# Kernel tuning notes

Hardware: AMD Instinct MI355X
Metric: run time of the kernel (lower is better)

## Reference

```python
import jax, jax.numpy as jnp
import numpy as np

HEADS = 4
C = 128            # per-head out channels (hard-coded 128 in the module)
NEG_SLOPE_ATT = 0.2   # GATConv attention leaky_relu slope
NEG_SLOPE = 0.01      # F.leaky_relu default slope


def _diag_output_ids(num_groups, n):
    # ids = base_i + n*j + j for group i, agent j; base_i = i * n^2
    i = np.arange(num_groups)[:, None] * (n * n)
    j = np.arange(n)[None, :] * (n + 1)
    return jnp.asarray((i + j).reshape(-1))


def setup_inputs() -> dict:
    key = jax.random.key(0)
    ks = jax.random.split(key, 12)
    num_groups, n_agents = 12, 48
    N = num_groups * n_agents * n_agents      # 27648 nodes
    E = 442368
    F_in, edge_dim, hidden = 256, 16, 256
    s = 0.05
    return {
        "x": jax.random.normal(ks[0], (N, F_in), jnp.float32),
        "edge_index": jax.random.randint(ks[1], (2, E), 0, N, jnp.int32),
        "edge_attr": jax.random.normal(ks[2], (E, edge_dim), jnp.float32),
        "num_groups": num_groups,
        "agents_per_group": n_agents,
        "W": jax.random.normal(ks[3], (F_in, HEADS * C), jnp.float32) * s,
        "att_src": jax.random.normal(ks[4], (HEADS, C), jnp.float32) * s,
        "att_dst": jax.random.normal(ks[5], (HEADS, C), jnp.float32) * s,
        "W_edge": jax.random.normal(ks[6], (edge_dim, HEADS * C), jnp.float32) * s,
        "att_edge": jax.random.normal(ks[7], (HEADS, C), jnp.float32) * s,
        "bias_gat": jnp.zeros((HEADS * C,), jnp.float32),
        "fc_W": jax.random.normal(ks[8], (HEADS * C, hidden), jnp.float32) * s,
        "fc_b": jnp.zeros((hidden,), jnp.float32),
    }


def _gat_conv(x, src, dst, edge_attr_full, W, att_src, att_dst, W_edge, att_edge, bias):
    N = x.shape[0]
    h = (x @ W).reshape(N, HEADS, C)                       # [N,H,C]
    a_src = jnp.einsum('nhc,hc->nh', h, att_src)           # [N,H]
    a_dst = jnp.einsum('nhc,hc->nh', h, att_dst)
    he = (edge_attr_full @ W_edge).reshape(-1, HEADS, C)   # [E',H,C]
    a_edge = jnp.einsum('ehc,hc->eh', he, att_edge)
    logits = jax.nn.leaky_relu(a_src[src] + a_dst[dst] + a_edge, NEG_SLOPE_ATT)
    # segment softmax over incoming edges of each dst node
    m = jax.ops.segment_max(logits, dst, num_segments=N)   # [N,H]
    e = jnp.exp(logits - m[dst])
    s = jax.ops.segment_sum(e, dst, num_segments=N)
    alpha = e / (s[dst] + 1e-16)                           # [E',H]
    msg = h[src] * alpha[..., None]                        # [E',H,C]
    out = jax.ops.segment_sum(msg, dst, num_segments=N)    # [N,H,C]
    return out.reshape(N, HEADS * C) + bias


def reference(x, edge_index, edge_attr, num_groups, agents_per_group,
              W, att_src, att_dst, W_edge, att_edge, bias_gat, fc_W, fc_b):
    N = x.shape[0]
    # add self-loops (PyG default), self-loop edge_attr = mean fill
    loops = jnp.arange(N, dtype=edge_index.dtype)
    src = jnp.concatenate([edge_index[0], loops])
    dst = jnp.concatenate([edge_index[1], loops])
    ea = jnp.concatenate([edge_attr,
                          jnp.broadcast_to(edge_attr.mean(0), (N, edge_attr.shape[1]))])
    h = jax.nn.leaky_relu(
        _gat_conv(x, src, dst, ea, W, att_src, att_dst, W_edge, att_edge, bias_gat),
        NEG_SLOPE)
    ids = _diag_output_ids(num_groups, agents_per_group)
    # fc_output + leaky_relu then diagonal index-select (select first: same math)
    return jax.nn.leaky_relu(h[ids] @ fc_W + fc_b, NEG_SLOPE)
```

## Files before the change

### kernel.cpp

```cpp
#include <hip/hip_runtime.h>

#define NNODES 27648
#define NEDGES 442368
#define FIN    256
#define HC     512
#define NH     4
#define CDIM   128
#define NAG    48
#define NGRP   12
#define N2     2304
#define NOUT   576
#define CAP    128
#define EDIM   16
#define MPART  512
#define BINB0  (9 + MPART)
#define PREB   (BINB0 + NEDGES/256)


__device__ __forceinline__ float lrelu(float v, float s){ return v > 0.0f ? v : s * v; }

__device__ __forceinline__ float wsum(float v){
  #pragma unroll
  for (int off = 32; off; off >>= 1) v += __shfl_xor(v, off, 64);
  return v;
}
__device__ __forceinline__ float wmax(float v){
  #pragma unroll
  for (int off = 32; off; off >>= 1) v = fmaxf(v, __shfl_xor(v, off, 64));
  return v;
}

__global__ __launch_bounds__(256) void k_pre(
    const float* __restrict__ W, const float* __restrict__ att_src,
    const float* __restrict__ att_dst, const float* __restrict__ W_edge,
    const float* __restrict__ att_edge, const float* __restrict__ ea,
    const int* __restrict__ ei,
    float* __restrict__ ws_, float* __restrict__ wd_, float* __restrict__ we_,
    float* __restrict__ easum, int* __restrict__ counts, int* __restrict__ slist){
  int b = blockIdx.x;
  int tid = threadIdx.x;
  if (b < 9) {
    int g = b * 256 + tid;
    if (g < 1024) {
      int f = g >> 2, h = g & 3;
      const float4* wp = (const float4*)(W + f*HC + h*CDIM);
      const float4* ap = (const float4*)(att_src + h*CDIM);
      float s = 0.f;
      #pragma unroll 8
      for (int c4 = 0; c4 < CDIM/4; c4++){
        float4 wv = wp[c4], av = ap[c4];
        s += wv.x*av.x + wv.y*av.y + wv.z*av.z + wv.w*av.w;
      }
      ws_[g] = s;
    } else if (g < 2048) {
      int gg = g - 1024; int f = gg >> 2, h = gg & 3;
      const float4* wp = (const float4*)(W + f*HC + h*CDIM);
      const float4* ap = (const float4*)(att_dst + h*CDIM);
      float s = 0.f;
      #pragma unroll 8
      for (int c4 = 0; c4 < CDIM/4; c4++){
        float4 wv = wp[c4], av = ap[c4];
        s += wv.x*av.x + wv.y*av.y + wv.z*av.z + wv.w*av.w;
      }
      wd_[gg] = s;
    } else if (g < 2112) {
      int gg = g - 2048; int d = gg >> 2, h = gg & 3;
      const float4* wp = (const float4*)(W_edge + d*HC + h*CDIM);
      const float4* ap = (const float4*)(att_edge + h*CDIM);
      float s = 0.f;
      #pragma unroll 8
      for (int c4 = 0; c4 < CDIM/4; c4++){
        float4 wv = wp[c4], av = ap[c4];
        s += wv.x*av.x + wv.y*av.y + wv.z*av.z + wv.w*av.w;
      }
      we_[gg] = s;
    }
  } else if (b < BINB0) {
    int pb = b - 9;
    const float4* p = (const float4*)ea;
    const int total = NEDGES * 4;
    float4 acc = make_float4(0.f, 0.f, 0.f, 0.f);
    for (int i = pb*256 + tid; i < total; i += MPART*256){
      float4 v = p[i];
      acc.x += v.x; acc.y += v.y; acc.z += v.z; acc.w += v.w;
    }
    #pragma unroll
    for (int off = 4; off <= 32; off <<= 1){
      acc.x += __shfl_xor(acc.x, off, 64);
      acc.y += __shfl_xor(acc.y, off, 64);
      acc.z += __shfl_xor(acc.z, off, 64);
      acc.w += __shfl_xor(acc.w, off, 64);
    }
    __shared__ float4 sd4[16];
    int lane = tid & 63, wave = tid >> 6;
    if (lane < 4) sd4[wave*4 + lane] = acc;
    __syncthreads();
    if (tid < 4){
      float4 t = sd4[tid];
      float4 a = sd4[4+tid], c = sd4[8+tid], d = sd4[12+tid];
      t.x += a.x + c.x + d.x; t.y += a.y + c.y + d.y;
      t.z += a.z + c.z + d.z; t.w += a.w + c.w + d.w;
      atomicAdd(&easum[4*tid+0], t.x);
      atomicAdd(&easum[4*tid+1], t.y);
      atomicAdd(&easum[4*tid+2], t.z);
      atomicAdd(&easum[4*tid+3], t.w);
    }
  } else {
    int e = (b - BINB0)*256 + tid;
    int dst = ei[NEDGES + e];
    int r = dst % N2;
    if (r % 49) return;
    int row = (dst / N2) * NAG + r / 49;
    int pos = atomicAdd(&counts[row], 1);
    if (pos >= CAP) return;
    slist[row*CAP + pos] = e;
  }
}

__global__ __launch_bounds__(256) void k_attn(const float* __restrict__ x,
    const int* __restrict__ ei, const float* __restrict__ ea,
    const float* __restrict__ ws_, const float* __restrict__ wd_,
    const float* __restrict__ we_, const float* __restrict__ easum,
    const int* __restrict__ counts, const int* __restrict__ slist,
    float* __restrict__ z){
  __shared__ float  lg[(CAP+1)*4];
  __shared__ int    srcs[CAP+1];
  __shared__ float  adst_s[4];
  __shared__ float4 pz[4*256];
  int row = blockIdx.x;
  int tid = threadIdx.x;
  int lane = tid & 63, wave = tid >> 6;
  int k = counts[row]; if (k > CAP) k = CAP;
  int g = row / NAG, j = row - g*NAG;
  int dst = g*N2 + j*49;

  float wsr[4][4];
  #pragma unroll
  for (int q = 0; q < 4; q++){
    float4 t = *(const float4*)(ws_ + (lane*4+q)*4);
    wsr[q][0]=t.x; wsr[q][1]=t.y; wsr[q][2]=t.z; wsr[q][3]=t.w;
  }
  float4 we4 = (lane < 16) ? *(const float4*)(we_ + lane*4)
                           : make_float4(0.f,0.f,0.f,0.f);

  for (int i = wave; i < k; i += 4){
    int e = slist[row*CAP + i];
    int src = ei[e];
    float eav = (lane < 16) ? ea[(size_t)e*EDIM + lane] : 0.f;
    float4 xv = *(const float4*)(x + (size_t)src*FIN + lane*4);
    float p0 = xv.x*wsr[0][0] + xv.y*wsr[1][0] + xv.z*wsr[2][0] + xv.w*wsr[3][0] + eav*we4.x;
    float p1 = xv.x*wsr[0][1] + xv.y*wsr[1][1] + xv.z*wsr[2][1] + xv.w*wsr[3][1] + eav*we4.y;
    float p2 = xv.x*wsr[0][2] + xv.y*wsr[1][2] + xv.z*wsr[2][2] + xv.w*wsr[3][2] + eav*we4.z;
    float p3 = xv.x*wsr[0][3] + xv.y*wsr[1][3] + xv.z*wsr[2][3] + xv.w*wsr[3][3] + eav*we4.w;
    p0 = wsum(p0); p1 = wsum(p1); p2 = wsum(p2); p3 = wsum(p3);
    if (lane == 0){
      srcs[i] = src;
      lg[i*4+0] = p0; lg[i*4+1] = p1; lg[i*4+2] = p2; lg[i*4+3] = p3;
    }
  }

  if (wave == 0){
    float wdr[4][4];
    #pragma unroll
    for (int q = 0; q < 4; q++){
      float4 t = *(const float4*)(wd_ + (lane*4+q)*4);
      wdr[q][0]=t.x; wdr[q][1]=t.y; wdr[q][2]=t.z; wdr[q][3]=t.w;
    }
    float4 xv = *(const float4*)(x + (size_t)dst*FIN + lane*4);
    const float invE = 1.0f/(float)NEDGES;
    float c = (lane < 16) ? easum[lane]*invE : 0.f;
    float ps[4], pd[4];
    ps[0] = xv.x*wsr[0][0] + xv.y*wsr[1][0] + xv.z*wsr[2][0] + xv.w*wsr[3][0] + c*we4.x;
    ps[1] = xv.x*wsr[0][1] + xv.y*wsr[1][1] + xv.z*wsr[2][1] + xv.w*wsr[3][1] + c*we4.y;
    ps[2] = xv.x*wsr[0][2] + xv.y*wsr[1][2] + xv.z*wsr[2][2] + xv.w*wsr[3][2] + c*we4.z;
    ps[3] = xv.x*wsr[0][3] + xv.y*wsr[1][3] + xv.z*wsr[2][3] + xv.w*wsr[3][3] + c*we4.w;
    #pragma unroll
    for (int h = 0; h < 4; h++){
      pd[h] = xv.x*wdr[0][h] + xv.y*wdr[1][h] + xv.z*wdr[2][h] + xv.w*wdr[3][h];
      ps[h] = wsum(ps[h]);
      pd[h] = wsum(pd[h]);
    }
    if (lane == 0){
      #pragma unroll
      for (int h = 0; h < 4; h++){
        adst_s[h] = pd[h];
        lg[k*4+h] = ps[h];
      }
      srcs[k] = dst;
    }
  }
  __syncthreads();

  {
    int h = wave;
    float ad = adst_s[h];
    float m = -1e30f;
    for (int i = lane; i <= k; i += 64){
      float v = lrelu(lg[i*4+h] + ad, 0.2f);
      lg[i*4+h] = v;
      m = fmaxf(m, v);
    }
    m = wmax(m);
    float s = 0.f;
    for (int i = lane; i <= k; i += 64){
      float e = __expf(lg[i*4+h] - m);
      lg[i*4+h] = e;
      s += e;
    }
    s = wsum(s);
    float inv = 1.0f/(s + 1e-16f);
    for (int i = lane; i <= k; i += 64) lg[i*4+h] *= inv;
  }
  __syncthreads();

  {
    float acc[4][4];
    #pragma unroll
    for (int h = 0; h < 4; h++)
      #pragma unroll
      for (int c = 0; c < 4; c++) acc[h][c] = 0.f;
    for (int i = wave; i <= k; i += 4){
      int src = srcs[i];
      float4 xv = *(const float4*)(x + (size_t)src*FIN + lane*4);
      float a0 = lg[i*4+0], a1 = lg[i*4+1], a2 = lg[i*4+2], a3 = lg[i*4+3];
      acc[0][0] += a0*xv.x; acc[0][1] += a0*xv.y; acc[0][2] += a0*xv.z; acc[0][3] += a0*xv.w;
      acc[1][0] += a1*xv.x; acc[1][1] += a1*xv.y; acc[1][2] += a1*xv.z; acc[1][3] += a1*xv.w;
      acc[2][0] += a2*xv.x; acc[2][1] += a2*xv.y; acc[2][2] += a2*xv.z; acc[2][3] += a2*xv.w;
      acc[3][0] += a3*xv.x; acc[3][1] += a3*xv.y; acc[3][2] += a3*xv.z; acc[3][3] += a3*xv.w;
    }
    #pragma unroll
    for (int h = 0; h < 4; h++)
      pz[wave*256 + h*64 + lane] =
        make_float4(acc[h][0], acc[h][1], acc[h][2], acc[h][3]);
  }
  __syncthreads();
  {
    float4 a = pz[tid], b = pz[256+tid], c = pz[512+tid], d = pz[768+tid];
    ((float4*)(z + (size_t)row*1024))[tid] =
      make_float4(a.x+b.x+c.x+d.x, a.y+b.y+c.y+d.y,
                  a.z+b.z+c.z+d.z, a.w+b.w+c.w+d.w);
  }
}

__global__ __launch_bounds__(256) void k_gemm1(const float* __restrict__ z,
    const float* __restrict__ W, const float* __restrict__ bias,
    float* __restrict__ h2){
  __shared__ float  zt[256][8];
  __shared__ float4 part[8][8][32];
  int rb = blockIdx.x * 8;
  int h  = blockIdx.y;
  int tid = threadIdx.x;
  for (int idx = tid; idx < 2048; idx += 256){
    int r = idx >> 8, f = idx & 255;
    zt[f][r] = z[(size_t)(rb+r)*1024 + h*256 + f];
  }
  __syncthreads();
  {
    int cg = tid & 31, q = tid >> 5;
    const float4* Wp = (const float4*)(W + h*CDIM) + cg;
    float4 acc[8];
    #pragma unroll
    for (int r = 0; r < 8; r++) acc[r] = make_float4(0.f,0.f,0.f,0.f);
    int f0 = q*32;
    #pragma unroll 8
    for (int jf = 0; jf < 32; jf++){
      int f = f0 + jf;
      float4 w4 = Wp[(size_t)f*(HC/4)];
      float4 zlo = *(const float4*)&zt[f][0];
      float4 zhi = *(const float4*)&zt[f][4];
      acc[0].x += zlo.x*w4.x; acc[0].y += zlo.x*w4.y; acc[0].z += zlo.x*w4.z; acc[0].w += zlo.x*w4.w;
      acc[1].x += zlo.y*w4.x; acc[1].y += zlo.y*w4.y; acc[1].z += zlo.y*w4.z; acc[1].w += zlo.y*w4.w;
      acc[2].x += zlo.z*w4.x; acc[2].y += zlo.z*w4.y; acc[2].z += zlo.z*w4.z; acc[2].w += zlo.z*w4.w;
      acc[3].x += zlo.w*w4.x; acc[3].y += zlo.w*w4.y; acc[3].z += zlo.w*w4.z; acc[3].w += zlo.w*w4.w;
      acc[4].x += zhi.x*w4.x; acc[4].y += zhi.x*w4.y; acc[4].z += zhi.x*w4.z; acc[4].w += zhi.x*w4.w;
      acc[5].x += zhi.y*w4.x; acc[5].y += zhi.y*w4.y; acc[5].z += zhi.y*w4.z; acc[5].w += zhi.y*w4.w;
      acc[6].x += zhi.z*w4.x; acc[6].y += zhi.z*w4.y; acc[6].z += zhi.z*w4.z; acc[6].w += zhi.z*w4.w;
      acc[7].x += zhi.w*w4.x; acc[7].y += zhi.w*w4.y; acc[7].z += zhi.w*w4.z; acc[7].w += zhi.w*w4.w;
    }
    #pragma unroll
    for (int r = 0; r < 8; r++) part[q][r][cg] = acc[r];
  }
  __syncthreads();
  {
    int r = tid >> 5, cg = tid & 31;
    float4 s0 = part[0][r][cg];
    #pragma unroll
    for (int q = 1; q < 8; q++){
      float4 t = part[q][r][cg];
      s0.x += t.x; s0.y += t.y; s0.z += t.z; s0.w += t.w;
    }
    float4 bs = ((const float4*)bias)[h*32 + cg];
    float4 o;
    o.x = lrelu(s0.x+bs.x, 0.01f);
    o.y = lrelu(s0.y+bs.y, 0.01f);
    o.z = lrelu(s0.z+bs.z, 0.01f);
    o.w = lrelu(s0.w+bs.w, 0.01f);
    *(float4*)(h2 + (size_t)(rb+r)*HC + h*CDIM + 4*cg) = o;
  }
}

__global__ __launch_bounds__(256) void k_gemm2(const float* __restrict__ h2,
    const float* __restrict__ fcW, const float* __restrict__ fcb,
    float* __restrict__ out){
  __shared__ float  ht[512][8];
  __shared__ float4 part[16][8][16];
  int rb = blockIdx.x * 8;
  int cb = blockIdx.y;
  int tid = threadIdx.x;
  for (int idx = tid; idx < 4096; idx += 256){
    int r = idx >> 9, kf = idx & 511;
    ht[kf][r] = h2[(size_t)(rb+r)*HC + kf];
  }
  __syncthreads();
  {
    int cg = tid & 15, q = tid >> 4;
    const float4* Fp = (const float4*)(fcW + cb*64) + cg;
    float4 acc[8];
    #pragma unroll
    for (int r = 0; r < 8; r++) acc[r] = make_float4(0.f,0.f,0.f,0.f);
    int k0 = q*32;
    #pragma unroll 8
    for (int jk = 0; jk < 32; jk++){
      int kf = k0 + jk;
      float4 w4 = Fp[(size_t)kf*64];
      float4 hlo = *(const float4*)&ht[kf][0];
      float4 hhi = *(const float4*)&ht[kf][4];
      acc[0].x += hlo.x*w4.x; acc[0].y += hlo.x*w4.y; acc[0].z += hlo.x*w4.z; acc[0].w += hlo.x*w4.w;
      acc[1].x += hlo.y*w4.x; acc[1].y += hlo.y*w4.y; acc[1].z += hlo.y*w4.z; acc[1].w += hlo.y*w4.w;
      acc[2].x += hlo.z*w4.x; acc[2].y += hlo.z*w4.y; acc[2].z += hlo.z*w4.z; acc[2].w += hlo.z*w4.w;
      acc[3].x += hlo.w*w4.x; acc[3].y += hlo.w*w4.y; acc[3].z += hlo.w*w4.z; acc[3].w += hlo.w*w4.w;
      acc[4].x += hhi.x*w4.x; acc[4].y += hhi.x*w4.y; acc[4].z += hhi.x*w4.z; acc[4].w += hhi.x*w4.w;
      acc[5].x += hhi.y*w4.x; acc[5].y += hhi.y*w4.y; acc[5].z += hhi.y*w4.z; acc[5].w += hhi.y*w4.w;
      acc[6].x += hhi.z*w4.x; acc[6].y += hhi.z*w4.y; acc[6].z += hhi.z*w4.z; acc[6].w += hhi.z*w4.w;
      acc[7].x += hhi.w*w4.x; acc[7].y += hhi.w*w4.y; acc[7].z += hhi.w*w4.z; acc[7].w += hhi.w*w4.w;
    }
    #pragma unroll
    for (int r = 0; r < 8; r++) part[q][r][cg] = acc[r];
  }
  __syncthreads();
  if (tid < 128){
    int r = tid >> 4, cg = tid & 15;
    float4 s0 = part[0][r][cg];
    #pragma unroll
    for (int q = 1; q < 16; q++){
      float4 t = part[q][r][cg];
      s0.x += t.x; s0.y += t.y; s0.z += t.z; s0.w += t.w;
    }
    float4 bs = ((const float4*)fcb)[cb*16 + cg];
    float4 o;
    o.x = lrelu(s0.x+bs.x, 0.01f);
    o.y = lrelu(s0.y+bs.y, 0.01f);
    o.z = lrelu(s0.z+bs.z, 0.01f);
    o.w = lrelu(s0.w+bs.w, 0.01f);
    *(float4*)(out + (size_t)(rb+r)*256 + cb*64 + 4*cg) = o;
  }
}

extern "C" void kernel_launch(void* const* d_in, const int* in_sizes, int n_in,
                              void* d_out, int out_size, void* d_ws, size_t ws_size,
                              hipStream_t stream) {
  const float* x        = (const float*)d_in[0];
  const int*   ei       = (const int*)  d_in[1];
  const float* ea       = (const float*)d_in[2];
  const float* W        = (const float*)d_in[5];
  const float* att_src  = (const float*)d_in[6];
  const float* att_dst  = (const float*)d_in[7];
  const float* W_edge   = (const float*)d_in[8];
  const float* att_edge = (const float*)d_in[9];
  const float* bias     = (const float*)d_in[10];
  const float* fcW      = (const float*)d_in[11];
  const float* fcb      = (const float*)d_in[12];
  float* out = (float*)d_out;

  float* w = (float*)d_ws;
  float*  ws_       = w;
  float*  wd_       = w + 1024;
  float*  we_       = w + 2048;
  float*  easum     = w + 2112;
  int*    counts    = (int*)(w + 2128);
  int*    slist     = (int*)(w + 2704);
  float*  z         = w + 76432;
  float*  h2        = w + 666256;

  hipMemsetAsync(easum, 0, (16 + NOUT)*sizeof(float), stream);
  k_pre<<<PREB, 256, 0, stream>>>(W, att_src, att_dst, W_edge, att_edge, ea, ei,
                                  ws_, wd_, we_, easum, counts, slist);
  k_attn<<<NOUT, 256, 0, stream>>>(x, ei, ea, ws_, wd_, we_, easum,
                                   counts, slist, z);
  k_gemm1<<<dim3(NOUT/8, 4), 256, 0, stream>>>(z, W, bias, h2);
  k_gemm2<<<dim3(NOUT/8, 4), 256, 0, stream>>>(h2, fcW, fcb, out);
}
```

Measured before the change: 167.9 us.

## Split edge binning into scan kernel, precompute edge logits, widen attention blocks

The memset is removed: counts are now zeroed inside k_pre, and the edge_attr sum is written as per-block partials instead of using atomics. A new k_scan kernel bins edges by destination, stores the source id directly, and precomputes the per-edge attention term from edge_attr, while one extra block reduces the partial sums. k_attn runs with 512 threads (8 waves) and reads the precomputed edge logits, which removes the indirect ei/ea gathers. In exchange this adds a kernel launch and a serial dependency, and the 8-way partial reduction makes shared memory larger.

```diff
diff --git a/kernel.cpp b/kernel.cpp
--- a/kernel.cpp
+++ b/kernel.cpp
@@ -13,8 +13,6 @@
 #define CAP    128
 #define EDIM   16
 #define MPART  512
-#define BINB0  (9 + MPART)
-#define PREB   (BINB0 + NEDGES/256)
 
 
 __device__ __forceinline__ float lrelu(float v, float s){ return v > 0.0f ? v : s * v; }
@@ -34,12 +32,11 @@
     const float* __restrict__ W, const float* __restrict__ att_src,
     const float* __restrict__ att_dst, const float* __restrict__ W_edge,
     const float* __restrict__ att_edge, const float* __restrict__ ea,
-    const int* __restrict__ ei,
     float* __restrict__ ws_, float* __restrict__ wd_, float* __restrict__ we_,
-    float* __restrict__ easum, int* __restrict__ counts, int* __restrict__ slist){
+    int* __restrict__ counts, float4* __restrict__ easum_part){
   int b = blockIdx.x;
   int tid = threadIdx.x;
-  if (b < 9) {
+  if (b < 11) {
     int g = b * 256 + tid;
     if (g < 1024) {
       int f = g >> 2, h = g & 3;
@@ -74,9 +71,11 @@
         s += wv.x*av.x + wv.y*av.y + wv.z*av.z + wv.w*av.w;
       }
       we_[gg] = s;
-    }
-  } else if (b < BINB0) {
-    int pb = b - 9;
+    } else if (g < 2112 + NOUT) {
+      counts[g - 2112] = 0;
+    }
+  } else {
+    int pb = b - 11;
     const float4* p = (const float4*)ea;
     const int total = NEDGES * 4;
     float4 acc = make_float4(0.f, 0.f, 0.f, 0.f);
@@ -100,33 +99,60 @@
       float4 a = sd4[4+tid], c = sd4[8+tid], d = sd4[12+tid];
       t.x += a.x + c.x + d.x; t.y += a.y + c.y + d.y;
       t.z += a.z + c.z + d.z; t.w += a.w + c.w + d.w;
-      atomicAdd(&easum[4*tid+0], t.x);
-      atomicAdd(&easum[4*tid+1], t.y);
-      atomicAdd(&easum[4*tid+2], t.z);
-      atomicAdd(&easum[4*tid+3], t.w);
-    }
-  } else {
-    int e = (b - BINB0)*256 + tid;
-    int dst = ei[NEDGES + e];
-    int r = dst % N2;
-    if (r % 49) return;
-    int row = (dst / N2) * NAG + r / 49;
-    int pos = atomicAdd(&counts[row], 1);
-    if (pos >= CAP) return;
-    slist[row*CAP + pos] = e;
-  }
-}
-
-__global__ __launch_bounds__(256) void k_attn(const float* __restrict__ x,
-    const int* __restrict__ ei, const float* __restrict__ ea,
+      easum_part[pb*4 + tid] = t;
+    }
+  }
+}
+
+__global__ __launch_bounds__(256) void k_scan(const int* __restrict__ ei,
+    const float* __restrict__ ea, const float* __restrict__ we_,
+    int* __restrict__ counts, int* __restrict__ slist, float* __restrict__ aed,
+    const float* __restrict__ easum_part, float* __restrict__ easum){
+  int tid = threadIdx.x;
+  if (blockIdx.x == NEDGES/256){
+    int col = tid & 15, part = tid >> 4;
+    float s = 0.f;
+    for (int pb = 0; pb < MPART/16; pb++)
+      s += easum_part[(part*(MPART/16) + pb)*16 + col];
+    __shared__ float sd[256];
+    sd[tid] = s;
+    __syncthreads();
+    if (tid < 16){
+      float t = 0.f;
+      #pragma unroll
+      for (int i = 0; i < 16; i++) t += sd[i*16 + tid];
+      easum[tid] = t;
+    }
+    return;
+  }
+  int e = blockIdx.x*256 + tid;
+  int dst = ei[NEDGES + e];
+  int r = dst % N2;
+  if (r % 49) return;
+  int row = (dst / N2) * NAG + r / 49;
+  int pos = atomicAdd(&counts[row], 1);
+  if (pos >= CAP) return;
+  slist[row*CAP + pos] = ei[e];
+  const float* eap = ea + (size_t)e*EDIM;
+  float a0=0.f,a1=0.f,a2=0.f,a3=0.f;
+  #pragma unroll
+  for (int d = 0; d < EDIM; d++){
+    float v = eap[d];
+    a0 += v*we_[d*4+0]; a1 += v*we_[d*4+1]; a2 += v*we_[d*4+2]; a3 += v*we_[d*4+3];
+  }
+  float* ap = aed + (size_t)(row*CAP+pos)*4;
+  ap[0]=a0; ap[1]=a1; ap[2]=a2; ap[3]=a3;
+}
+
+__global__ __launch_bounds__(512) void k_attn(const float* __restrict__ x,
     const float* __restrict__ ws_, const float* __restrict__ wd_,
     const float* __restrict__ we_, const float* __restrict__ easum,
     const int* __restrict__ counts, const int* __restrict__ slist,
-    float* __restrict__ z){
+    const float* __restrict__ aed, float* __restrict__ z){
   __shared__ float  lg[(CAP+1)*4];
   __shared__ int    srcs[CAP+1];
   __shared__ float  adst_s[4];
-  __shared__ float4 pz[4*256];
+  __shared__ float4 pz[8*256];
   int row = blockIdx.x;
   int tid = threadIdx.x;
   int lane = tid & 63, wave = tid >> 6;
@@ -140,22 +166,20 @@
     float4 t = *(const float4*)(ws_ + (lane*4+q)*4);
     wsr[q][0]=t.x; wsr[q][1]=t.y; wsr[q][2]=t.z; wsr[q][3]=t.w;
   }
-  float4 we4 = (lane < 16) ? *(const float4*)(we_ + lane*4)
-                           : make_float4(0.f,0.f,0.f,0.f);
-
-  for (int i = wave; i < k; i += 4){
-    int e = slist[row*CAP + i];
-    int src = ei[e];
-    float eav = (lane < 16) ? ea[(size_t)e*EDIM + lane] : 0.f;
+
+  for (int i = wave; i < k; i += 8){
+    int src = slist[row*CAP + i];
+    float4 aedv = *(const float4*)(aed + (size_t)(row*CAP+i)*4);
     float4 xv = *(const float4*)(x + (size_t)src*FIN + lane*4);
-    float p0 = xv.x*wsr[0][0] + xv.y*wsr[1][0] + xv.z*wsr[2][0] + xv.w*wsr[3][0] + eav*we4.x;
-    float p1 = xv.x*wsr[0][1] + xv.y*wsr[1][1] + xv.z*wsr[2][1] + xv.w*wsr[3][1] + eav*we4.y;
-    float p2 = xv.x*wsr[0][2] + xv.y*wsr[1][2] + xv.z*wsr[2][2] + xv.w*wsr[3][2] + eav*we4.z;
-    float p3 = xv.x*wsr[0][3] + xv.y*wsr[1][3] + xv.z*wsr[2][3] + xv.w*wsr[3][3] + eav*we4.w;
+    float p0 = xv.x*wsr[0][0] + xv.y*wsr[1][0] + xv.z*wsr[2][0] + xv.w*wsr[3][0];
+    float p1 = xv.x*wsr[0][1] + xv.y*wsr[1][1] + xv.z*wsr[2][1] + xv.w*wsr[3][1];
+    float p2 = xv.x*wsr[0][2] + xv.y*wsr[1][2] + xv.z*wsr[2][2] + xv.w*wsr[3][2];
+    float p3 = xv.x*wsr[0][3] + xv.y*wsr[1][3] + xv.z*wsr[2][3] + xv.w*wsr[3][3];
     p0 = wsum(p0); p1 = wsum(p1); p2 = wsum(p2); p3 = wsum(p3);
     if (lane == 0){
       srcs[i] = src;
-      lg[i*4+0] = p0; lg[i*4+1] = p1; lg[i*4+2] = p2; lg[i*4+3] = p3;
+      lg[i*4+0] = p0 + aedv.x; lg[i*4+1] = p1 + aedv.y;
+      lg[i*4+2] = p2 + aedv.z; lg[i*4+3] = p3 + aedv.w;
     }
   }
 
@@ -167,31 +191,34 @@
       wdr[q][0]=t.x; wdr[q][1]=t.y; wdr[q][2]=t.z; wdr[q][3]=t.w;
     }
     float4 xv = *(const float4*)(x + (size_t)dst*FIN + lane*4);
-    const float invE = 1.0f/(float)NEDGES;
-    float c = (lane < 16) ? easum[lane]*invE : 0.f;
-    float ps[4], pd[4];
-    ps[0] = xv.x*wsr[0][0] + xv.y*wsr[1][0] + xv.z*wsr[2][0] + xv.w*wsr[3][0] + c*we4.x;
-    ps[1] = xv.x*wsr[0][1] + xv.y*wsr[1][1] + xv.z*wsr[2][1] + xv.w*wsr[3][1] + c*we4.y;
-    ps[2] = xv.x*wsr[0][2] + xv.y*wsr[1][2] + xv.z*wsr[2][2] + xv.w*wsr[3][2] + c*we4.z;
-    ps[3] = xv.x*wsr[0][3] + xv.y*wsr[1][3] + xv.z*wsr[2][3] + xv.w*wsr[3][3] + c*we4.w;
+    float pd[4], ps[4];
     #pragma unroll
     for (int h = 0; h < 4; h++){
       pd[h] = xv.x*wdr[0][h] + xv.y*wdr[1][h] + xv.z*wdr[2][h] + xv.w*wdr[3][h];
+      ps[h] = xv.x*wsr[0][h] + xv.y*wsr[1][h] + xv.z*wsr[2][h] + xv.w*wsr[3][h];
+    }
+    const float invE = 1.0f/(float)NEDGES;
+    float md = (lane < 16) ? easum[lane]*invE : 0.f;
+    float al[4];
+    #pragma unroll
+    for (int h = 0; h < 4; h++){
+      float c = (lane < 16) ? md*we_[lane*4+h] : 0.f;
+      al[h] = wsum(c);
+      pd[h] = wsum(pd[h]);
       ps[h] = wsum(ps[h]);
-      pd[h] = wsum(pd[h]);
     }
     if (lane == 0){
       #pragma unroll
       for (int h = 0; h < 4; h++){
         adst_s[h] = pd[h];
-        lg[k*4+h] = ps[h];
+        lg[k*4+h] = ps[h] + al[h];
       }
       srcs[k] = dst;
     }
   }
   __syncthreads();
 
-  {
+  if (wave < 4){
     int h = wave;
     float ad = adst_s[h];
     float m = -1e30f;
@@ -219,7 +246,7 @@
     for (int h = 0; h < 4; h++)
       #pragma unroll
       for (int c = 0; c < 4; c++) acc[h][c] = 0.f;
-    for (int i = wave; i <= k; i += 4){
+    for (int i = wave; i <= k; i += 8){
       int src = srcs[i];
       float4 xv = *(const float4*)(x + (size_t)src*FIN + lane*4);
       float a0 = lg[i*4+0], a1 = lg[i*4+1], a2 = lg[i*4+2], a3 = lg[i*4+3];
@@ -234,11 +261,14 @@
         make_float4(acc[h][0], acc[h][1], acc[h][2], acc[h][3]);
   }
   __syncthreads();
-  {
-    float4 a = pz[tid], b = pz[256+tid], c = pz[512+tid], d = pz[768+tid];
-    ((float4*)(z + (size_t)row*1024))[tid] =
-      make_float4(a.x+b.x+c.x+d.x, a.y+b.y+c.y+d.y,
-                  a.z+b.z+c.z+d.z, a.w+b.w+c.w+d.w);
+  if (tid < 256){
+    float4 s0 = pz[tid];
+    #pragma unroll
+    for (int w = 1; w < 8; w++){
+      float4 t = pz[w*256 + tid];
+      s0.x += t.x; s0.y += t.y; s0.z += t.z; s0.w += t.w;
+    }
+    ((float4*)(z + (size_t)row*1024))[tid] = s0;
   }
 }
 
@@ -378,15 +408,17 @@
   float*  we_       = w + 2048;
   float*  easum     = w + 2112;
   int*    counts    = (int*)(w + 2128);
-  int*    slist     = (int*)(w + 2704);
-  float*  z         = w + 76432;
-  float*  h2        = w + 666256;
-
-  hipMemsetAsync(easum, 0, (16 + NOUT)*sizeof(float), stream);
-  k_pre<<<PREB, 256, 0, stream>>>(W, att_src, att_dst, W_edge, att_edge, ea, ei,
-                                  ws_, wd_, we_, easum, counts, slist);
-  k_attn<<<NOUT, 256, 0, stream>>>(x, ei, ea, ws_, wd_, we_, easum,
-                                   counts, slist, z);
+  float*  easum_p   = w + 2704;
+  int*    slist     = (int*)(w + 10896);
+  float*  aed       = w + 84624;
+  float*  z         = w + 379536;
+  float*  h2        = w + 969360;
+
+  k_pre<<<11 + MPART, 256, 0, stream>>>(W, att_src, att_dst, W_edge, att_edge, ea,
+                                        ws_, wd_, we_, counts, (float4*)easum_p);
+  k_scan<<<NEDGES/256 + 1, 256, 0, stream>>>(ei, ea, we_, counts, slist, aed,
+                                             easum_p, easum);
+  k_attn<<<NOUT, 512, 0, stream>>>(x, ws_, wd_, we_, easum, counts, slist, aed, z);
   k_gemm1<<<dim3(NOUT/8, 4), 256, 0, stream>>>(z, W, bias, h2);
   k_gemm2<<<dim3(NOUT/8, 4), 256, 0, stream>>>(h2, fcW, fcb, out);
 }
```

After: 147.1 us, median of 2. -12.4%, faster.

## Double attention block width and precompute edge logits per edge in a batched pass

Applied to the files above, without the earlier changes.

The attention kernel now runs 512 threads (8 waves) per output row instead of 256. Each incoming edge's source index and edge-attribute logit contribution are computed once, one thread per edge, in a cooperative prologue and staged in shared memory. The gather loops then stride over 8 waves, and the final reduction sums 8 partial accumulators. This aims to expose more memory-level parallelism for the x-row gathers and to remove the serialized per-edge slist/ei/ea loads from the wave loop, at the cost of extra barriers, more shared memory and fewer blocks per CU.

```diff
diff --git a/kernel.cpp b/kernel.cpp
--- a/kernel.cpp
+++ b/kernel.cpp
@@ -13,8 +13,9 @@
 #define CAP    128
 #define EDIM   16
 #define MPART  512
-#define BINB0  (9 + MPART)
-#define PREB   (BINB0 + NEDGES/256)
+#define PRE_WB 9
+#define PRE_EB (PRE_WB + MPART)
+#define PREB   (PRE_EB + NEDGES/256)
 
 
 __device__ __forceinline__ float lrelu(float v, float s){ return v > 0.0f ? v : s * v; }
@@ -39,7 +40,7 @@
     float* __restrict__ easum, int* __restrict__ counts, int* __restrict__ slist){
   int b = blockIdx.x;
   int tid = threadIdx.x;
-  if (b < 9) {
+  if (b < PRE_WB) {
     int g = b * 256 + tid;
     if (g < 1024) {
       int f = g >> 2, h = g & 3;
@@ -75,8 +76,8 @@
       }
       we_[gg] = s;
     }
-  } else if (b < BINB0) {
-    int pb = b - 9;
+  } else if (b < PRE_EB) {
+    int pb = b - PRE_WB;
     const float4* p = (const float4*)ea;
     const int total = NEDGES * 4;
     float4 acc = make_float4(0.f, 0.f, 0.f, 0.f);
@@ -106,7 +107,7 @@
       atomicAdd(&easum[4*tid+3], t.w);
     }
   } else {
-    int e = (b - BINB0)*256 + tid;
+    int e = (b - PRE_EB)*256 + tid;
     int dst = ei[NEDGES + e];
     int r = dst % N2;
     if (r % 49) return;
@@ -117,7 +118,7 @@
   }
 }
 
-__global__ __launch_bounds__(256) void k_attn(const float* __restrict__ x,
+__global__ __launch_bounds__(512) void k_attn(const float* __restrict__ x,
     const int* __restrict__ ei, const float* __restrict__ ea,
     const float* __restrict__ ws_, const float* __restrict__ wd_,
     const float* __restrict__ we_, const float* __restrict__ easum,
@@ -126,7 +127,9 @@
   __shared__ float  lg[(CAP+1)*4];
   __shared__ int    srcs[CAP+1];
   __shared__ float  adst_s[4];
-  __shared__ float4 pz[4*256];
+  __shared__ float  wesh[64];
+  __shared__ float4 aedsh[CAP];
+  __shared__ float4 pz[8*256];
   int row = blockIdx.x;
   int tid = threadIdx.x;
   int lane = tid & 63, wave = tid >> 6;
@@ -134,28 +137,46 @@
   int g = row / NAG, j = row - g*NAG;
   int dst = g*N2 + j*49;
 
+  if (tid < 64) wesh[tid] = we_[tid];
+  __syncthreads();
+
+  if (tid < k){
+    int e = slist[row*CAP + tid];
+    int src = ei[e];
+    const float4* eap = (const float4*)(ea + (size_t)e*EDIM);
+    float4 e0 = eap[0], e1 = eap[1], e2 = eap[2], e3 = eap[3];
+    float a[4];
+    #pragma unroll
+    for (int h = 0; h < 4; h++){
+      a[h] = e0.x*wesh[0*4+h]  + e0.y*wesh[1*4+h]  + e0.z*wesh[2*4+h]  + e0.w*wesh[3*4+h]
+           + e1.x*wesh[4*4+h]  + e1.y*wesh[5*4+h]  + e1.z*wesh[6*4+h]  + e1.w*wesh[7*4+h]
+           + e2.x*wesh[8*4+h]  + e2.y*wesh[9*4+h]  + e2.z*wesh[10*4+h] + e2.w*wesh[11*4+h]
+           + e3.x*wesh[12*4+h] + e3.y*wesh[13*4+h] + e3.z*wesh[14*4+h] + e3.w*wesh[15*4+h];
+    }
+    srcs[tid] = src;
+    aedsh[tid] = make_float4(a[0], a[1], a[2], a[3]);
+  }
+  __syncthreads();
+
   float wsr[4][4];
   #pragma unroll
   for (int q = 0; q < 4; q++){
     float4 t = *(const float4*)(ws_ + (lane*4+q)*4);
     wsr[q][0]=t.x; wsr[q][1]=t.y; wsr[q][2]=t.z; wsr[q][3]=t.w;
   }
-  float4 we4 = (lane < 16) ? *(const float4*)(we_ + lane*4)
-                           : make_float4(0.f,0.f,0.f,0.f);
-
-  for (int i = wave; i < k; i += 4){
-    int e = slist[row*CAP + i];
-    int src = ei[e];
-    float eav = (lane < 16) ? ea[(size_t)e*EDIM + lane] : 0.f;
+
+  for (int i = wave; i < k; i += 8){
+    int src = srcs[i];
+    float4 aedv = aedsh[i];
     float4 xv = *(const float4*)(x + (size_t)src*FIN + lane*4);
-    float p0 = xv.x*wsr[0][0] + xv.y*wsr[1][0] + xv.z*wsr[2][0] + xv.w*wsr[3][0] + eav*we4.x;
-    float p1 = xv.x*wsr[0][1] + xv.y*wsr[1][1] + xv.z*wsr[2][1] + xv.w*wsr[3][1] + eav*we4.y;
-    float p2 = xv.x*wsr[0][2] + xv.y*wsr[1][2] + xv.z*wsr[2][2] + xv.w*wsr[3][2] + eav*we4.z;
-    float p3 = xv.x*wsr[0][3] + xv.y*wsr[1][3] + xv.z*wsr[2][3] + xv.w*wsr[3][3] + eav*we4.w;
+    float p0 = xv.x*wsr[0][0] + xv.y*wsr[1][0] + xv.z*wsr[2][0] + xv.w*wsr[3][0];
+    float p1 = xv.x*wsr[0][1] + xv.y*wsr[1][1] + xv.z*wsr[2][1] + xv.w*wsr[3][1];
+    float p2 = xv.x*wsr[0][2] + xv.y*wsr[1][2] + xv.z*wsr[2][2] + xv.w*wsr[3][2];
+    float p3 = xv.x*wsr[0][3] + xv.y*wsr[1][3] + xv.z*wsr[2][3] + xv.w*wsr[3][3];
     p0 = wsum(p0); p1 = wsum(p1); p2 = wsum(p2); p3 = wsum(p3);
     if (lane == 0){
-      srcs[i] = src;
-      lg[i*4+0] = p0; lg[i*4+1] = p1; lg[i*4+2] = p2; lg[i*4+3] = p3;
+      lg[i*4+0] = p0 + aedv.x; lg[i*4+1] = p1 + aedv.y;
+      lg[i*4+2] = p2 + aedv.z; lg[i*4+3] = p3 + aedv.w;
     }
   }
 
@@ -167,31 +188,34 @@
       wdr[q][0]=t.x; wdr[q][1]=t.y; wdr[q][2]=t.z; wdr[q][3]=t.w;
     }
     float4 xv = *(const float4*)(x + (size_t)dst*FIN + lane*4);
-    const float invE = 1.0f/(float)NEDGES;
-    float c = (lane < 16) ? easum[lane]*invE : 0.f;
-    float ps[4], pd[4];
-    ps[0] = xv.x*wsr[0][0] + xv.y*wsr[1][0] + xv.z*wsr[2][0] + xv.w*wsr[3][0] + c*we4.x;
-    ps[1] = xv.x*wsr[0][1] + xv.y*wsr[1][1] + xv.z*wsr[2][1] + xv.w*wsr[3][1] + c*we4.y;
-    ps[2] = xv.x*wsr[0][2] + xv.y*wsr[1][2] + xv.z*wsr[2][2] + xv.w*wsr[3][2] + c*we4.z;
-    ps[3] = xv.x*wsr[0][3] + xv.y*wsr[1][3] + xv.z*wsr[2][3] + xv.w*wsr[3][3] + c*we4.w;
+    float pd[4], ps[4];
     #pragma unroll
     for (int h = 0; h < 4; h++){
       pd[h] = xv.x*wdr[0][h] + xv.y*wdr[1][h] + xv.z*wdr[2][h] + xv.w*wdr[3][h];
+      ps[h] = xv.x*wsr[0][h] + xv.y*wsr[1][h] + xv.z*wsr[2][h] + xv.w*wsr[3][h];
+    }
+    const float invE = 1.0f/(float)NEDGES;
+    float md = (lane < 16) ? easum[lane]*invE : 0.f;
+    float al[4];
+    #pragma unroll
+    for (int h = 0; h < 4; h++){
+      float c = (lane < 16) ? md*wesh[lane*4+h] : 0.f;
+      al[h] = wsum(c);
+      pd[h] = wsum(pd[h]);
       ps[h] = wsum(ps[h]);
-      pd[h] = wsum(pd[h]);
     }
     if (lane == 0){
       #pragma unroll
       for (int h = 0; h < 4; h++){
         adst_s[h] = pd[h];
-        lg[k*4+h] = ps[h];
+        lg[k*4+h] = ps[h] + al[h];
       }
       srcs[k] = dst;
     }
   }
   __syncthreads();
 
-  {
+  if (wave < 4){
     int h = wave;
     float ad = adst_s[h];
     float m = -1e30f;
@@ -219,7 +243,7 @@
     for (int h = 0; h < 4; h++)
       #pragma unroll
       for (int c = 0; c < 4; c++) acc[h][c] = 0.f;
-    for (int i = wave; i <= k; i += 4){
+    for (int i = wave; i <= k; i += 8){
       int src = srcs[i];
       float4 xv = *(const float4*)(x + (size_t)src*FIN + lane*4);
       float a0 = lg[i*4+0], a1 = lg[i*4+1], a2 = lg[i*4+2], a3 = lg[i*4+3];
@@ -234,11 +258,14 @@
         make_float4(acc[h][0], acc[h][1], acc[h][2], acc[h][3]);
   }
   __syncthreads();
-  {
-    float4 a = pz[tid], b = pz[256+tid], c = pz[512+tid], d = pz[768+tid];
-    ((float4*)(z + (size_t)row*1024))[tid] =
-      make_float4(a.x+b.x+c.x+d.x, a.y+b.y+c.y+d.y,
-                  a.z+b.z+c.z+d.z, a.w+b.w+c.w+d.w);
+  if (tid < 256){
+    float4 s0 = pz[tid];
+    #pragma unroll
+    for (int w = 1; w < 8; w++){
+      float4 t = pz[w*256 + tid];
+      s0.x += t.x; s0.y += t.y; s0.z += t.z; s0.w += t.w;
+    }
+    ((float4*)(z + (size_t)row*1024))[tid] = s0;
   }
 }
 
@@ -385,7 +412,7 @@
   hipMemsetAsync(easum, 0, (16 + NOUT)*sizeof(float), stream);
   k_pre<<<PREB, 256, 0, stream>>>(W, att_src, att_dst, W_edge, att_edge, ea, ei,
                                   ws_, wd_, we_, easum, counts, slist);
-  k_attn<<<NOUT, 256, 0, stream>>>(x, ei, ea, ws_, wd_, we_, easum,
+  k_attn<<<NOUT, 512, 0, stream>>>(x, ei, ea, ws_, wd_, we_, easum,
                                    counts, slist, z);
   k_gemm1<<<dim3(NOUT/8, 4), 256, 0, stream>>>(z, W, bias, h2);
   k_gemm2<<<dim3(NOUT/8, 4), 256, 0, stream>>>(h2, fcW, fcb, out);
```

New measurement: 162.6 us. 3.1% less time.
